# Performance work log

Hardware: AMD Instinct MI355X
Metric: run time of the kernel (lower is better)

The kernel has to match this reference:

```python
import jax, jax.numpy as jnp
import numpy as np

ALPHA = 1.702  # sigmoid-GLU scale
LIMIT = 7.0    # clamp limit
TOP_K = 2      # num_experts_per_tok


def setup_inputs() -> dict:
    key = jax.random.key(0)
    ks = jax.random.split(key, 4)
    B, S, H, E, I = 2, 1024, 1024, 8, 2048
    return {
        "hidden_states": jax.random.normal(ks[0], (B, S, H), jnp.float32),
        "router_weight": jax.random.normal(ks[1], (E, H), jnp.float32),
        "router_bias": jnp.zeros((E,), jnp.float32),
        "gate_up_proj": jax.random.normal(ks[2], (E, H, 2 * I), jnp.float32) * 0.02,
        "gate_up_bias": jnp.zeros((E, 2 * I), jnp.float32),
        "down_proj": jax.random.normal(ks[3], (E, I, H), jnp.float32) * 0.02,
        "down_bias": jnp.zeros((E, H), jnp.float32),
    }


def reference(hidden_states, router_weight, router_bias, gate_up_proj,
              gate_up_bias, down_proj, down_bias):
    B, S, H = hidden_states.shape
    E, _, two_I = gate_up_proj.shape
    I = two_I // 2

    flat = hidden_states.reshape(B * S, H)  # [T, H]

    # Router: softmax + top-k
    logits = flat @ router_weight.T + router_bias            # [T, E]
    scores = jax.nn.softmax(logits, axis=-1)
    topk_w, topk_idx = jax.lax.top_k(scores, TOP_K)          # [T, K]

    # Dense per-expert gated FFN (einsum 'abmh,ehn->abemn' computes all experts
    # on all tokens; the reshape/permute dance is a mathematical no-op).
    gu = jnp.einsum('th,ehn->ten', flat, gate_up_proj) + gate_up_bias  # [T, E, 2I]
    gate = jnp.minimum(gu[..., :I], LIMIT)
    up = jnp.clip(gu[..., I:], -LIMIT, LIMIT)
    glu = gate * jax.nn.sigmoid(gate * ALPHA)
    act = (up + 1.0) * glu                                   # [T, E, I]

    down = jnp.einsum('tei,eih->teh', act, down_proj) + down_bias  # [T, E, H]

    # Combine: gather each token's top-k expert outputs, weighted sum.
    gathered = jnp.take_along_axis(down, topk_idx[:, :, None], axis=1)  # [T, K, H]
    out = (gathered * topk_w[:, :, None]).sum(axis=1)        # [T, H]
    return out.reshape(B, S, H)
```

## Files before the change

### kernel.cpp

```cpp
#include <hip/hip_runtime.h>
#include <math.h>

#define TT 2048
#define HH 1024
#define EE 8
#define II 2048
#define N1 4096
#define ALPHA 1.702f
#define LIMIT 7.0f

typedef __attribute__((ext_vector_type(8))) short short8;
typedef __attribute__((ext_vector_type(4))) float floatx4;

__device__ __forceinline__ short f2bf(float f) {
  union { float f; unsigned u; } v; v.f = f;
  unsigned r = (v.u + 0x7fffu + ((v.u >> 16) & 1u)) >> 16;
  return (short)r;
}
__device__ __forceinline__ float bf2f(unsigned short s) {
  union { unsigned u; float f; } v; v.u = ((unsigned)s) << 16;
  return v.f;
}

__global__ __launch_bounds__(256) void router_kernel(
    const float* __restrict__ x, const float* __restrict__ rw,
    const float* __restrict__ rb, int* __restrict__ topk_idx,
    float* __restrict__ topk_w) {
  const int t = blockIdx.x;
  const float* xr = x + (size_t)t * HH;
  const int lane = threadIdx.x & 63;
  const int wave = threadIdx.x >> 6;
  float xv[16];
#pragma unroll
  for (int i = 0; i < 16; i++) xv[i] = xr[lane + i * 64];
  __shared__ float logits[EE];
#pragma unroll
  for (int ee = 0; ee < 2; ee++) {
    const int e = wave * 2 + ee;
    const float* wr = rw + (size_t)e * HH;
    float s = 0.f;
#pragma unroll
    for (int i = 0; i < 16; i++) s += xv[i] * wr[lane + i * 64];
#pragma unroll
    for (int off = 32; off > 0; off >>= 1) s += __shfl_down(s, off, 64);
    if (lane == 0) logits[e] = s + rb[e];
  }
  __syncthreads();
  if (threadIdx.x == 0) {
    float l[EE], sc[EE];
    float mx = -3.4e38f;
    for (int i = 0; i < EE; i++) { l[i] = logits[i]; mx = fmaxf(mx, l[i]); }
    float sum = 0.f;
    for (int i = 0; i < EE; i++) { sc[i] = expf(l[i] - mx); sum += sc[i]; }
    const float inv = 1.f / sum;
    int i0 = 0;
    for (int i = 1; i < EE; i++) if (sc[i] > sc[i0]) i0 = i;
    int i1 = (i0 == 0) ? 1 : 0;
    for (int i = 0; i < EE; i++) if (i != i0 && sc[i] > sc[i1]) i1 = i;
    topk_idx[t * 2 + 0] = i0;
    topk_idx[t * 2 + 1] = i1;
    topk_w[t * 2 + 0] = sc[i0] * inv;
    topk_w[t * 2 + 1] = sc[i1] * inv;
  }
}

__global__ void assign_kernel(const int* __restrict__ topk_idx,
                              int* __restrict__ counts, int* __restrict__ rows) {
  const int id = blockIdx.x * blockDim.x + threadIdx.x;
  if (id >= TT * 2) return;
  const int e = topk_idx[id];
  const int slot = atomicAdd(&counts[e], 1);
  rows[e * TT + slot] = id;
}

__global__ __launch_bounds__(256) void gemm_gu(
    const float* __restrict__ x, const float* __restrict__ gup,
    const float* __restrict__ gub, const int* __restrict__ counts,
    const int* __restrict__ rows, unsigned short* __restrict__ gu) {
  const int e = blockIdx.z, mtile = blockIdx.y, ntile = blockIdx.x;
  const int count = counts[e];
  if (mtile * 128 >= count) return;
  const int* rl = rows + e * TT + mtile * 128;
  __shared__ short As[128][40];
  __shared__ short Bs[128][40];
  const int tid = threadIdx.x;
  const int lane = tid & 63, wave = tid >> 6;
  const int wm = (wave & 1) << 6, wn = (wave >> 1) << 6;
  const int quad = lane >> 4, r16 = lane & 15;

  const int arow = tid >> 2, akoct = tid & 3;
  const int cr0 = (mtile * 128 + arow < count) ? arow : (count - 1 - mtile * 128);
  const int cr1 = (mtile * 128 + arow + 64 < count) ? arow + 64 : (count - 1 - mtile * 128);
  const float* a0 = x + (size_t)(rl[cr0] >> 1) * HH;
  const float* a1 = x + (size_t)(rl[cr1] >> 1) * HH;

  const int bn = tid & 127, bk = tid >> 7;
  const float* bb = gup + (size_t)e * HH * N1 + ntile * 128 + bn;

  floatx4 acc[4][4] = {};

  for (int k0 = 0; k0 < HH; k0 += 32) {
    __syncthreads();
    {
      const float4* p = (const float4*)(a0 + k0 + akoct * 8);
      float4 v0 = p[0], v1 = p[1];
      short8 s;
      s[0]=f2bf(v0.x); s[1]=f2bf(v0.y); s[2]=f2bf(v0.z); s[3]=f2bf(v0.w);
      s[4]=f2bf(v1.x); s[5]=f2bf(v1.y); s[6]=f2bf(v1.z); s[7]=f2bf(v1.w);
      *(short8*)&As[arow][akoct * 8] = s;
      p = (const float4*)(a1 + k0 + akoct * 8);
      v0 = p[0]; v1 = p[1];
      s[0]=f2bf(v0.x); s[1]=f2bf(v0.y); s[2]=f2bf(v0.z); s[3]=f2bf(v0.w);
      s[4]=f2bf(v1.x); s[5]=f2bf(v1.y); s[6]=f2bf(v1.z); s[7]=f2bf(v1.w);
      *(short8*)&As[arow + 64][akoct * 8] = s;
    }
    {
      const float* p = bb + (size_t)(k0 + bk * 8) * N1;
      short8 s;
#pragma unroll
      for (int j = 0; j < 8; j++) s[j] = f2bf(p[(size_t)j * N1]);
      *(short8*)&Bs[bn][bk * 8] = s;
      p = bb + (size_t)(k0 + (bk + 2) * 8) * N1;
#pragma unroll
      for (int j = 0; j < 8; j++) s[j] = f2bf(p[(size_t)j * N1]);
      *(short8*)&Bs[bn][(bk + 2) * 8] = s;
    }
    __syncthreads();
    short8 af[4], bf_[4];
#pragma unroll
    for (int i = 0; i < 4; i++)
      af[i] = *(const short8*)&As[wm + i * 16 + r16][quad * 8];
#pragma unroll
    for (int j = 0; j < 4; j++)
      bf_[j] = *(const short8*)&Bs[wn + j * 16 + r16][quad * 8];
#pragma unroll
    for (int i = 0; i < 4; i++)
#pragma unroll
      for (int j = 0; j < 4; j++)
        acc[i][j] = __builtin_amdgcn_mfma_f32_16x16x32_bf16(af[i], bf_[j], acc[i][j], 0, 0, 0);
  }
#pragma unroll
  for (int i = 0; i < 4; i++) {
#pragma unroll
    for (int reg = 0; reg < 4; reg++) {
      const int rrow = wm + i * 16 + quad * 4 + reg;
      if (mtile * 128 + rrow < count) {
        const int ent = rl[rrow];
        unsigned short* orow = gu + (size_t)ent * N1 + ntile * 128;
#pragma unroll
        for (int j = 0; j < 4; j++) {
          const int c = wn + j * 16 + r16;
          const float v = acc[i][j][reg] + gub[e * N1 + ntile * 128 + c];
          orow[c] = (unsigned short)f2bf(v);
        }
      }
    }
  }
}

__global__ void act_kernel(const unsigned short* __restrict__ gu,
                           unsigned short* __restrict__ act) {
  const int id = blockIdx.x * blockDim.x + threadIdx.x;
  if (id >= TT * 2 * II) return;
  const int r = id >> 11;
  const int i = id & (II - 1);
  float g = bf2f(gu[(size_t)r * N1 + i]);
  float u = bf2f(gu[(size_t)r * N1 + II + i]);
  g = fminf(g, LIMIT);
  u = fminf(fmaxf(u, -LIMIT), LIMIT);
  const float glu = g / (1.f + expf(-g * ALPHA));
  act[(size_t)r * II + i] = (unsigned short)f2bf((u + 1.f) * glu);
}

__global__ __launch_bounds__(256) void gemm_down(
    const unsigned short* __restrict__ act, const float* __restrict__ dp,
    const float* __restrict__ db, const int* __restrict__ counts,
    const int* __restrict__ rows, float* __restrict__ dout) {
  const int e = blockIdx.z, mtile = blockIdx.y, ntile = blockIdx.x;
  const int count = counts[e];
  if (mtile * 128 >= count) return;
  const int* rl = rows + e * TT + mtile * 128;
  __shared__ short As[128][40];
  __shared__ short Bs[128][40];
  const int tid = threadIdx.x;
  const int lane = tid & 63, wave = tid >> 6;
  const int wm = (wave & 1) << 6, wn = (wave >> 1) << 6;
  const int quad = lane >> 4, r16 = lane & 15;

  const int arow = tid >> 2, akoct = tid & 3;
  const int cr0 = (mtile * 128 + arow < count) ? arow : (count - 1 - mtile * 128);
  const int cr1 = (mtile * 128 + arow + 64 < count) ? arow + 64 : (count - 1 - mtile * 128);
  const unsigned short* a0 = act + (size_t)rl[cr0] * II;
  const unsigned short* a1 = act + (size_t)rl[cr1] * II;

  const int bn = tid & 127, bk = tid >> 7;
  const float* bb = dp + (size_t)e * II * HH + ntile * 128 + bn;

  floatx4 acc[4][4] = {};

  for (int k0 = 0; k0 < II; k0 += 32) {
    __syncthreads();
    {
      *(short8*)&As[arow][akoct * 8] = *(const short8*)(a0 + k0 + akoct * 8);
      *(short8*)&As[arow + 64][akoct * 8] = *(const short8*)(a1 + k0 + akoct * 8);
    }
    {
      const float* p = bb + (size_t)(k0 + bk * 8) * HH;
      short8 s;
#pragma unroll
      for (int j = 0; j < 8; j++) s[j] = f2bf(p[(size_t)j * HH]);
      *(short8*)&Bs[bn][bk * 8] = s;
      p = bb + (size_t)(k0 + (bk + 2) * 8) * HH;
#pragma unroll
      for (int j = 0; j < 8; j++) s[j] = f2bf(p[(size_t)j * HH]);
      *(short8*)&Bs[bn][(bk + 2) * 8] = s;
    }
    __syncthreads();
    short8 af[4], bf_[4];
#pragma unroll
    for (int i = 0; i < 4; i++)
      af[i] = *(const short8*)&As[wm + i * 16 + r16][quad * 8];
#pragma unroll
    for (int j = 0; j < 4; j++)
      bf_[j] = *(const short8*)&Bs[wn + j * 16 + r16][quad * 8];
#pragma unroll
    for (int i = 0; i < 4; i++)
#pragma unroll
      for (int j = 0; j < 4; j++)
        acc[i][j] = __builtin_amdgcn_mfma_f32_16x16x32_bf16(af[i], bf_[j], acc[i][j], 0, 0, 0);
  }
#pragma unroll
  for (int i = 0; i < 4; i++) {
#pragma unroll
    for (int reg = 0; reg < 4; reg++) {
      const int rrow = wm + i * 16 + quad * 4 + reg;
      if (mtile * 128 + rrow < count) {
        const int ent = rl[rrow];
        float* orow = dout + (size_t)ent * HH + ntile * 128;
#pragma unroll
        for (int j = 0; j < 4; j++) {
          const int c = wn + j * 16 + r16;
          orow[c] = acc[i][j][reg] + db[e * HH + ntile * 128 + c];
        }
      }
    }
  }
}

__global__ void combine_kernel(const float* __restrict__ dout,
                               const float* __restrict__ tw,
                               float* __restrict__ out) {
  const int id = blockIdx.x * blockDim.x + threadIdx.x;
  const int t = id >> 8;
  const int h = (id & 255) * 4;
  const float w0 = tw[t * 2], w1 = tw[t * 2 + 1];
  const float4 a = *(const float4*)(dout + (size_t)(2 * t) * HH + h);
  const float4 b = *(const float4*)(dout + (size_t)(2 * t + 1) * HH + h);
  float4 o;
  o.x = w0 * a.x + w1 * b.x;
  o.y = w0 * a.y + w1 * b.y;
  o.z = w0 * a.z + w1 * b.z;
  o.w = w0 * a.w + w1 * b.w;
  *(float4*)(out + (size_t)t * HH + h) = o;
}

extern "C" void kernel_launch(void* const* d_in, const int* in_sizes, int n_in,
                              void* d_out, int out_size, void* d_ws, size_t ws_size,
                              hipStream_t stream) {
  const float* x   = (const float*)d_in[0];
  const float* rw  = (const float*)d_in[1];
  const float* rb  = (const float*)d_in[2];
  const float* gup = (const float*)d_in[3];
  const float* gub = (const float*)d_in[4];
  const float* dp  = (const float*)d_in[5];
  const float* db  = (const float*)d_in[6];
  float* out = (float*)d_out;

  char* ws = (char*)d_ws;
  int*   topk_idx = (int*)(ws + 0);
  float* topk_w   = (float*)(ws + 16384);
  int*   counts   = (int*)(ws + 32768);
  int*   rows     = (int*)(ws + 33024);
  unsigned short* gu  = (unsigned short*)(ws + 131072);
  unsigned short* act = (unsigned short*)(ws + 131072 + 33554432);
  float* dout = (float*)(ws + 131072 + 33554432 + 16777216);

  router_kernel<<<TT, 256, 0, stream>>>(x, rw, rb, topk_idx, topk_w);
  hipMemsetAsync(counts, 0, 64, stream);
  assign_kernel<<<(TT * 2 + 255) / 256, 256, 0, stream>>>(topk_idx, counts, rows);
  gemm_gu<<<dim3(N1 / 128, TT / 128, EE), 256, 0, stream>>>(x, gup, gub, counts, rows, gu);
  act_kernel<<<(TT * 2 * II) / 256, 256, 0, stream>>>(gu, act);
  gemm_down<<<dim3(HH / 128, TT / 128, EE), 256, 0, stream>>>(act, dp, db, counts, rows, dout);
  combine_kernel<<<(TT * HH / 4) / 256, 256, 0, stream>>>(dout, topk_w, out);
}
```

Measured before the change: 454.3 us.

## Pre-transpose weights to bf16, pipeline GEMMs with async LDS loads, fuse activation

Adds kernels that convert x to bf16 and transpose both expert weight tensors into K-contiguous bf16 layouts each call. The GEMMs then stage tiles with global_load_lds in a double-buffered pipeline, avoiding strided fp32 loads and per-element conversion. gemm_gu now pairs gate and up columns in one tile and applies the GLU activation in its epilogue, which removes act_kernel and the gu intermediate. gemm_down splits K four ways into separate partial buffers that combine_kernel sums, trading more combine traffic for more parallel blocks. The per-call weight transpose adds memory traffic of its own.

```diff
diff --git a/kernel.cpp b/kernel.cpp
--- a/kernel.cpp
+++ b/kernel.cpp
@@ -11,15 +11,64 @@
 
 typedef __attribute__((ext_vector_type(8))) short short8;
 typedef __attribute__((ext_vector_type(4))) float floatx4;
+typedef __attribute__((ext_vector_type(4))) unsigned int uintx4;
 
 __device__ __forceinline__ short f2bf(float f) {
   union { float f; unsigned u; } v; v.f = f;
   unsigned r = (v.u + 0x7fffu + ((v.u >> 16) & 1u)) >> 16;
   return (short)r;
 }
-__device__ __forceinline__ float bf2f(unsigned short s) {
-  union { unsigned u; float f; } v; v.u = ((unsigned)s) << 16;
-  return v.f;
+__device__ __forceinline__ unsigned cvt2(float lo, float hi) {
+  unsigned r;
+  asm("v_cvt_pk_bf16_f32 %0, %1, %2" : "=v"(r) : "v"(lo), "v"(hi));
+  return r;
+}
+__device__ __forceinline__ void gload16(const void* g, void* l) {
+  __builtin_amdgcn_global_load_lds(
+      (const __attribute__((address_space(1))) unsigned int*)g,
+      (__attribute__((address_space(3))) unsigned int*)l, 16, 0, 0);
+}
+
+__global__ __launch_bounds__(256) void convert_x(const float* __restrict__ x,
+                                                 unsigned short* __restrict__ xb) {
+  const int id = blockIdx.x * 256 + threadIdx.x;
+  const float4 a = ((const float4*)x)[id * 2];
+  const float4 b = ((const float4*)x)[id * 2 + 1];
+  uintx4 w;
+  w[0] = cvt2(a.x, a.y); w[1] = cvt2(a.z, a.w);
+  w[2] = cvt2(b.x, b.y); w[3] = cvt2(b.z, b.w);
+  ((uintx4*)xb)[id] = w;
+}
+
+__global__ __launch_bounds__(256) void transpose_bf16(
+    const float* __restrict__ src, unsigned short* __restrict__ dst,
+    const int K, const int N) {
+  const int e = blockIdx.z;
+  const int n0 = blockIdx.x * 64, k0 = blockIdx.y * 64;
+  __shared__ float tile[64][68];
+  const float* s = src + (size_t)e * K * N;
+  unsigned short* d = dst + (size_t)e * N * K;
+  const int t = threadIdx.x;
+  const int nq = t & 15, kr = t >> 4;
+#pragma unroll
+  for (int r = 0; r < 4; r++) {
+    const int k = r * 16 + kr;
+    const float4 v = *(const float4*)(s + (size_t)(k0 + k) * N + n0 + nq * 4);
+    tile[k][nq * 4 + 0] = v.x; tile[k][nq * 4 + 1] = v.y;
+    tile[k][nq * 4 + 2] = v.z; tile[k][nq * 4 + 3] = v.w;
+  }
+  __syncthreads();
+  const int n = t >> 2, ks = (t & 3) * 16;
+  unsigned short* orow = d + (size_t)(n0 + n) * K + k0 + ks;
+  uintx4 w0, w1;
+#pragma unroll
+  for (int m = 0; m < 4; m++)
+    w0[m] = cvt2(tile[ks + 2 * m][n], tile[ks + 2 * m + 1][n]);
+#pragma unroll
+  for (int m = 0; m < 4; m++)
+    w1[m] = cvt2(tile[ks + 8 + 2 * m][n], tile[ks + 9 + 2 * m][n]);
+  *(uintx4*)orow = w0;
+  *(uintx4*)(orow + 8) = w1;
 }
 
 __global__ __launch_bounds__(256) void router_kernel(
@@ -73,178 +122,219 @@
   rows[e * TT + slot] = id;
 }
 
-__global__ __launch_bounds__(256) void gemm_gu(
-    const float* __restrict__ x, const float* __restrict__ gup,
+__global__ __launch_bounds__(256, 4) void gemm_gu(
+    const unsigned short* __restrict__ xb, const unsigned short* __restrict__ gupt,
     const float* __restrict__ gub, const int* __restrict__ counts,
-    const int* __restrict__ rows, unsigned short* __restrict__ gu) {
+    const int* __restrict__ rows, unsigned short* __restrict__ act) {
   const int e = blockIdx.z, mtile = blockIdx.y, ntile = blockIdx.x;
   const int count = counts[e];
   if (mtile * 128 >= count) return;
   const int* rl = rows + e * TT + mtile * 128;
-  __shared__ short As[128][40];
-  __shared__ short Bs[128][40];
+  __shared__ __align__(16) char smem[33280];
+  unsigned short* As = (unsigned short*)smem;
+  unsigned short* Bs = (unsigned short*)(smem + 16384);
+  float* glds = (float*)smem;
   const int tid = threadIdx.x;
   const int lane = tid & 63, wave = tid >> 6;
   const int wm = (wave & 1) << 6, wn = (wave >> 1) << 6;
   const int quad = lane >> 4, r16 = lane & 15;
 
-  const int arow = tid >> 2, akoct = tid & 3;
-  const int cr0 = (mtile * 128 + arow < count) ? arow : (count - 1 - mtile * 128);
-  const int cr1 = (mtile * 128 + arow + 64 < count) ? arow + 64 : (count - 1 - mtile * 128);
-  const float* a0 = x + (size_t)(rl[cr0] >> 1) * HH;
-  const float* a1 = x + (size_t)(rl[cr1] >> 1) * HH;
-
-  const int bn = tid & 127, bk = tid >> 7;
-  const float* bb = gup + (size_t)e * HH * N1 + ntile * 128 + bn;
+  const int lrow = lane >> 2, lko = (lane & 3) * 8;
+  const int q0 = wave * 2, q1 = q0 + 1;
+  const int row0 = q0 * 16 + lrow, row1 = q1 * 16 + lrow;
+  const int last = count - 1 - mtile * 128;
+  const int cr0 = row0 <= last ? row0 : last;
+  const int cr1 = row1 <= last ? row1 : last;
+  const unsigned short* pA0 = xb + (size_t)(rl[cr0] >> 1) * HH + lko;
+  const unsigned short* pA1 = xb + (size_t)(rl[cr1] >> 1) * HH + lko;
+  const int bn0 = (row0 < 64) ? (ntile * 64 + row0) : (II + ntile * 64 + row0 - 64);
+  const int bn1 = (row1 < 64) ? (ntile * 64 + row1) : (II + ntile * 64 + row1 - 64);
+  const unsigned short* pB0 = gupt + (size_t)e * N1 * HH + (size_t)bn0 * HH + lko;
+  const unsigned short* pB1 = gupt + (size_t)e * N1 * HH + (size_t)bn1 * HH + lko;
+  unsigned short* dA0 = As + q0 * 512;
+  unsigned short* dA1 = As + q1 * 512;
+  unsigned short* dB0 = Bs + q0 * 512;
+  unsigned short* dB1 = Bs + q1 * 512;
 
   floatx4 acc[4][4] = {};
-
-  for (int k0 = 0; k0 < HH; k0 += 32) {
-    __syncthreads();
-    {
-      const float4* p = (const float4*)(a0 + k0 + akoct * 8);
-      float4 v0 = p[0], v1 = p[1];
-      short8 s;
-      s[0]=f2bf(v0.x); s[1]=f2bf(v0.y); s[2]=f2bf(v0.z); s[3]=f2bf(v0.w);
-      s[4]=f2bf(v1.x); s[5]=f2bf(v1.y); s[6]=f2bf(v1.z); s[7]=f2bf(v1.w);
-      *(short8*)&As[arow][akoct * 8] = s;
-      p = (const float4*)(a1 + k0 + akoct * 8);
-      v0 = p[0]; v1 = p[1];
-      s[0]=f2bf(v0.x); s[1]=f2bf(v0.y); s[2]=f2bf(v0.z); s[3]=f2bf(v0.w);
-      s[4]=f2bf(v1.x); s[5]=f2bf(v1.y); s[6]=f2bf(v1.z); s[7]=f2bf(v1.w);
-      *(short8*)&As[arow + 64][akoct * 8] = s;
+  const int NTK = HH / 32;
+
+#define STAGE(B, kk) do { \
+    const int ko_ = (kk) * 32; \
+    gload16(pA0 + ko_, dA0 + (B) * 4096); \
+    gload16(pA1 + ko_, dA1 + (B) * 4096); \
+    gload16(pB0 + ko_, dB0 + (B) * 4096); \
+    gload16(pB1 + ko_, dB1 + (B) * 4096); \
+  } while (0)
+
+#define PHASE(B) do { \
+    asm volatile("s_waitcnt vmcnt(4)" ::: "memory"); \
+    __builtin_amdgcn_s_barrier(); \
+    short8 af[4], bf4[4]; \
+    _Pragma("unroll") for (int i = 0; i < 4; i++) \
+      af[i] = *(const short8*)(As + (B) * 4096 + (wm + i * 16 + r16) * 32 + quad * 8); \
+    _Pragma("unroll") for (int j = 0; j < 4; j++) \
+      bf4[j] = *(const short8*)(Bs + (B) * 4096 + (wn + j * 16 + r16) * 32 + quad * 8); \
+    asm volatile("s_waitcnt lgkmcnt(0)" ::: "memory"); \
+    __builtin_amdgcn_sched_barrier(0); \
+    __builtin_amdgcn_s_barrier(); \
+    { const int ks_ = kn < NTK ? kn : NTK - 1; kn++; STAGE(B, ks_); } \
+    __builtin_amdgcn_sched_barrier(0); \
+    __builtin_amdgcn_s_setprio(1); \
+    _Pragma("unroll") for (int i = 0; i < 4; i++) \
+      _Pragma("unroll") for (int j = 0; j < 4; j++) \
+        acc[i][j] = __builtin_amdgcn_mfma_f32_16x16x32_bf16(af[i], bf4[j], acc[i][j], 0, 0, 0); \
+    __builtin_amdgcn_s_setprio(0); \
+  } while (0)
+
+  STAGE(0, 0);
+  STAGE(1, 1);
+  int kn = 2;
+#pragma unroll 1
+  for (int t = 0; t < NTK; t += 2) {
+    PHASE(0);
+    PHASE(1);
+  }
+  asm volatile("s_waitcnt vmcnt(0)" ::: "memory");
+  __builtin_amdgcn_s_barrier();
+
+  const int colbase = ntile * 64;
+  if (wn == 0) {
+#pragma unroll
+    for (int j = 0; j < 4; j++) {
+      const int c = j * 16 + r16;
+      const float gb = gub[e * N1 + colbase + c];
+#pragma unroll
+      for (int i = 0; i < 4; i++)
+#pragma unroll
+        for (int reg = 0; reg < 4; reg++) {
+          const int rr = wm + i * 16 + quad * 4 + reg;
+          float g = acc[i][j][reg] + gb;
+          g = fminf(g, LIMIT);
+          glds[rr * 65 + c] = g / (1.f + expf(-g * ALPHA));
+        }
     }
-    {
-      const float* p = bb + (size_t)(k0 + bk * 8) * N1;
-      short8 s;
-#pragma unroll
-      for (int j = 0; j < 8; j++) s[j] = f2bf(p[(size_t)j * N1]);
-      *(short8*)&Bs[bn][bk * 8] = s;
-      p = bb + (size_t)(k0 + (bk + 2) * 8) * N1;
-#pragma unroll
-      for (int j = 0; j < 8; j++) s[j] = f2bf(p[(size_t)j * N1]);
-      *(short8*)&Bs[bn][(bk + 2) * 8] = s;
+  }
+  __builtin_amdgcn_s_barrier();
+  if (wn == 64) {
+#pragma unroll
+    for (int j = 0; j < 4; j++) {
+      const int c = j * 16 + r16;
+      const float ub = gub[e * N1 + II + colbase + c];
+#pragma unroll
+      for (int i = 0; i < 4; i++)
+#pragma unroll
+        for (int reg = 0; reg < 4; reg++) {
+          const int rr = wm + i * 16 + quad * 4 + reg;
+          if (mtile * 128 + rr < count) {
+            float u = acc[i][j][reg] + ub;
+            u = fminf(fmaxf(u, -LIMIT), LIMIT);
+            const float glu = glds[rr * 65 + c];
+            act[(size_t)rl[rr] * II + colbase + c] = (unsigned short)f2bf((u + 1.f) * glu);
+          }
+        }
     }
-    __syncthreads();
-    short8 af[4], bf_[4];
-#pragma unroll
-    for (int i = 0; i < 4; i++)
-      af[i] = *(const short8*)&As[wm + i * 16 + r16][quad * 8];
-#pragma unroll
-    for (int j = 0; j < 4; j++)
-      bf_[j] = *(const short8*)&Bs[wn + j * 16 + r16][quad * 8];
-#pragma unroll
-    for (int i = 0; i < 4; i++)
-#pragma unroll
-      for (int j = 0; j < 4; j++)
-        acc[i][j] = __builtin_amdgcn_mfma_f32_16x16x32_bf16(af[i], bf_[j], acc[i][j], 0, 0, 0);
-  }
-#pragma unroll
-  for (int i = 0; i < 4; i++) {
-#pragma unroll
-    for (int reg = 0; reg < 4; reg++) {
-      const int rrow = wm + i * 16 + quad * 4 + reg;
-      if (mtile * 128 + rrow < count) {
-        const int ent = rl[rrow];
-        unsigned short* orow = gu + (size_t)ent * N1 + ntile * 128;
-#pragma unroll
-        for (int j = 0; j < 4; j++) {
-          const int c = wn + j * 16 + r16;
-          const float v = acc[i][j][reg] + gub[e * N1 + ntile * 128 + c];
-          orow[c] = (unsigned short)f2bf(v);
-        }
-      }
-    }
-  }
-}
-
-__global__ void act_kernel(const unsigned short* __restrict__ gu,
-                           unsigned short* __restrict__ act) {
-  const int id = blockIdx.x * blockDim.x + threadIdx.x;
-  if (id >= TT * 2 * II) return;
-  const int r = id >> 11;
-  const int i = id & (II - 1);
-  float g = bf2f(gu[(size_t)r * N1 + i]);
-  float u = bf2f(gu[(size_t)r * N1 + II + i]);
-  g = fminf(g, LIMIT);
-  u = fminf(fmaxf(u, -LIMIT), LIMIT);
-  const float glu = g / (1.f + expf(-g * ALPHA));
-  act[(size_t)r * II + i] = (unsigned short)f2bf((u + 1.f) * glu);
-}
-
-__global__ __launch_bounds__(256) void gemm_down(
-    const unsigned short* __restrict__ act, const float* __restrict__ dp,
+  }
+#undef STAGE
+#undef PHASE
+}
+
+__global__ __launch_bounds__(256, 4) void gemm_down(
+    const unsigned short* __restrict__ act, const unsigned short* __restrict__ dpt,
     const float* __restrict__ db, const int* __restrict__ counts,
     const int* __restrict__ rows, float* __restrict__ dout) {
-  const int e = blockIdx.z, mtile = blockIdx.y, ntile = blockIdx.x;
+  const int e = blockIdx.z >> 2, kc = blockIdx.z & 3;
+  const int mtile = blockIdx.y, ntile = blockIdx.x;
   const int count = counts[e];
   if (mtile * 128 >= count) return;
+  const int kb = kc * (II / 4);
   const int* rl = rows + e * TT + mtile * 128;
-  __shared__ short As[128][40];
-  __shared__ short Bs[128][40];
+  __shared__ __align__(16) char smem[32768];
+  unsigned short* As = (unsigned short*)smem;
+  unsigned short* Bs = (unsigned short*)(smem + 16384);
   const int tid = threadIdx.x;
   const int lane = tid & 63, wave = tid >> 6;
   const int wm = (wave & 1) << 6, wn = (wave >> 1) << 6;
   const int quad = lane >> 4, r16 = lane & 15;
 
-  const int arow = tid >> 2, akoct = tid & 3;
-  const int cr0 = (mtile * 128 + arow < count) ? arow : (count - 1 - mtile * 128);
-  const int cr1 = (mtile * 128 + arow + 64 < count) ? arow + 64 : (count - 1 - mtile * 128);
-  const unsigned short* a0 = act + (size_t)rl[cr0] * II;
-  const unsigned short* a1 = act + (size_t)rl[cr1] * II;
-
-  const int bn = tid & 127, bk = tid >> 7;
-  const float* bb = dp + (size_t)e * II * HH + ntile * 128 + bn;
+  const int lrow = lane >> 2, lko = (lane & 3) * 8;
+  const int q0 = wave * 2, q1 = q0 + 1;
+  const int row0 = q0 * 16 + lrow, row1 = q1 * 16 + lrow;
+  const int last = count - 1 - mtile * 128;
+  const int cr0 = row0 <= last ? row0 : last;
+  const int cr1 = row1 <= last ? row1 : last;
+  const unsigned short* pA0 = act + (size_t)rl[cr0] * II + kb + lko;
+  const unsigned short* pA1 = act + (size_t)rl[cr1] * II + kb + lko;
+  const unsigned short* pB0 = dpt + (size_t)e * HH * II + (size_t)(ntile * 128 + row0) * II + kb + lko;
+  const unsigned short* pB1 = dpt + (size_t)e * HH * II + (size_t)(ntile * 128 + row1) * II + kb + lko;
+  unsigned short* dA0 = As + q0 * 512;
+  unsigned short* dA1 = As + q1 * 512;
+  unsigned short* dB0 = Bs + q0 * 512;
+  unsigned short* dB1 = Bs + q1 * 512;
 
   floatx4 acc[4][4] = {};
-
-  for (int k0 = 0; k0 < II; k0 += 32) {
-    __syncthreads();
-    {
-      *(short8*)&As[arow][akoct * 8] = *(const short8*)(a0 + k0 + akoct * 8);
-      *(short8*)&As[arow + 64][akoct * 8] = *(const short8*)(a1 + k0 + akoct * 8);
-    }
-    {
-      const float* p = bb + (size_t)(k0 + bk * 8) * HH;
-      short8 s;
-#pragma unroll
-      for (int j = 0; j < 8; j++) s[j] = f2bf(p[(size_t)j * HH]);
-      *(short8*)&Bs[bn][bk * 8] = s;
-      p = bb + (size_t)(k0 + (bk + 2) * 8) * HH;
-#pragma unroll
-      for (int j = 0; j < 8; j++) s[j] = f2bf(p[(size_t)j * HH]);
-      *(short8*)&Bs[bn][(bk + 2) * 8] = s;
-    }
-    __syncthreads();
-    short8 af[4], bf_[4];
-#pragma unroll
-    for (int i = 0; i < 4; i++)
-      af[i] = *(const short8*)&As[wm + i * 16 + r16][quad * 8];
-#pragma unroll
-    for (int j = 0; j < 4; j++)
-      bf_[j] = *(const short8*)&Bs[wn + j * 16 + r16][quad * 8];
-#pragma unroll
-    for (int i = 0; i < 4; i++)
-#pragma unroll
-      for (int j = 0; j < 4; j++)
-        acc[i][j] = __builtin_amdgcn_mfma_f32_16x16x32_bf16(af[i], bf_[j], acc[i][j], 0, 0, 0);
-  }
+  const int NTK = (II / 4) / 32;
+
+#define STAGE(B, kk) do { \
+    const int ko_ = (kk) * 32; \
+    gload16(pA0 + ko_, dA0 + (B) * 4096); \
+    gload16(pA1 + ko_, dA1 + (B) * 4096); \
+    gload16(pB0 + ko_, dB0 + (B) * 4096); \
+    gload16(pB1 + ko_, dB1 + (B) * 4096); \
+  } while (0)
+
+#define PHASE(B) do { \
+    asm volatile("s_waitcnt vmcnt(4)" ::: "memory"); \
+    __builtin_amdgcn_s_barrier(); \
+    short8 af[4], bf4[4]; \
+    _Pragma("unroll") for (int i = 0; i < 4; i++) \
+      af[i] = *(const short8*)(As + (B) * 4096 + (wm + i * 16 + r16) * 32 + quad * 8); \
+    _Pragma("unroll") for (int j = 0; j < 4; j++) \
+      bf4[j] = *(const short8*)(Bs + (B) * 4096 + (wn + j * 16 + r16) * 32 + quad * 8); \
+    asm volatile("s_waitcnt lgkmcnt(0)" ::: "memory"); \
+    __builtin_amdgcn_sched_barrier(0); \
+    __builtin_amdgcn_s_barrier(); \
+    { const int ks_ = kn < NTK ? kn : NTK - 1; kn++; STAGE(B, ks_); } \
+    __builtin_amdgcn_sched_barrier(0); \
+    __builtin_amdgcn_s_setprio(1); \
+    _Pragma("unroll") for (int i = 0; i < 4; i++) \
+      _Pragma("unroll") for (int j = 0; j < 4; j++) \
+        acc[i][j] = __builtin_amdgcn_mfma_f32_16x16x32_bf16(af[i], bf4[j], acc[i][j], 0, 0, 0); \
+    __builtin_amdgcn_s_setprio(0); \
+  } while (0)
+
+  STAGE(0, 0);
+  STAGE(1, 1);
+  int kn = 2;
+#pragma unroll 1
+  for (int t = 0; t < NTK; t += 2) {
+    PHASE(0);
+    PHASE(1);
+  }
+  asm volatile("s_waitcnt vmcnt(0)" ::: "memory");
+  __builtin_amdgcn_s_barrier();
+
+  float* dc = dout + (size_t)kc * ((size_t)TT * 2 * HH);
 #pragma unroll
   for (int i = 0; i < 4; i++) {
 #pragma unroll
     for (int reg = 0; reg < 4; reg++) {
-      const int rrow = wm + i * 16 + quad * 4 + reg;
-      if (mtile * 128 + rrow < count) {
-        const int ent = rl[rrow];
-        float* orow = dout + (size_t)ent * HH + ntile * 128;
+      const int rr = wm + i * 16 + quad * 4 + reg;
+      if (mtile * 128 + rr < count) {
+        const int ent = rl[rr];
+        float* orow = dc + (size_t)ent * HH + ntile * 128;
 #pragma unroll
         for (int j = 0; j < 4; j++) {
           const int c = wn + j * 16 + r16;
-          orow[c] = acc[i][j][reg] + db[e * HH + ntile * 128 + c];
+          float v = acc[i][j][reg];
+          if (kc == 0) v += db[e * HH + ntile * 128 + c];
+          orow[c] = v;
         }
       }
     }
   }
+#undef STAGE
+#undef PHASE
 }
 
 __global__ void combine_kernel(const float* __restrict__ dout,
@@ -254,8 +344,17 @@
   const int t = id >> 8;
   const int h = (id & 255) * 4;
   const float w0 = tw[t * 2], w1 = tw[t * 2 + 1];
-  const float4 a = *(const float4*)(dout + (size_t)(2 * t) * HH + h);
-  const float4 b = *(const float4*)(dout + (size_t)(2 * t + 1) * HH + h);
+  const size_t CH = (size_t)TT * 2 * HH;
+  const size_t r0 = (size_t)(2 * t) * HH + h;
+  const size_t r1 = (size_t)(2 * t + 1) * HH + h;
+  float4 a = {0.f, 0.f, 0.f, 0.f}, b = {0.f, 0.f, 0.f, 0.f};
+#pragma unroll
+  for (int c = 0; c < 4; c++) {
+    const float4 va = *(const float4*)(dout + c * CH + r0);
+    const float4 vb = *(const float4*)(dout + c * CH + r1);
+    a.x += va.x; a.y += va.y; a.z += va.z; a.w += va.w;
+    b.x += vb.x; b.y += vb.y; b.z += vb.z; b.w += vb.w;
+  }
   float4 o;
   o.x = w0 * a.x + w1 * b.x;
   o.y = w0 * a.y + w1 * b.y;
@@ -281,15 +380,19 @@
   float* topk_w   = (float*)(ws + 16384);
   int*   counts   = (int*)(ws + 32768);
   int*   rows     = (int*)(ws + 33024);
-  unsigned short* gu  = (unsigned short*)(ws + 131072);
-  unsigned short* act = (unsigned short*)(ws + 131072 + 33554432);
-  float* dout = (float*)(ws + 131072 + 33554432 + 16777216);
-
+  unsigned short* xb   = (unsigned short*)(ws + 131072);
+  unsigned short* gupt = (unsigned short*)(ws + 4325376);
+  unsigned short* dpt  = (unsigned short*)(ws + 71434240);
+  unsigned short* act  = (unsigned short*)(ws + 104988672);
+  float* dout = (float*)(ws + 4325376);
+
+  convert_x<<<TT * HH / 8 / 256, 256, 0, stream>>>(x, xb);
+  transpose_bf16<<<dim3(N1 / 64, HH / 64, EE), 256, 0, stream>>>(gup, gupt, HH, N1);
+  transpose_bf16<<<dim3(HH / 64, II / 64, EE), 256, 0, stream>>>(dp, dpt, II, HH);
   router_kernel<<<TT, 256, 0, stream>>>(x, rw, rb, topk_idx, topk_w);
   hipMemsetAsync(counts, 0, 64, stream);
   assign_kernel<<<(TT * 2 + 255) / 256, 256, 0, stream>>>(topk_idx, counts, rows);
-  gemm_gu<<<dim3(N1 / 128, TT / 128, EE), 256, 0, stream>>>(x, gup, gub, counts, rows, gu);
-  act_kernel<<<(TT * 2 * II) / 256, 256, 0, stream>>>(gu, act);
-  gemm_down<<<dim3(HH / 128, TT / 128, EE), 256, 0, stream>>>(act, dp, db, counts, rows, dout);
+  gemm_gu<<<dim3(II / 64, TT / 128, EE), 256, 0, stream>>>(xb, gupt, gub, counts, rows, act);
+  gemm_down<<<dim3(HH / 128, TT / 128, EE * 4), 256, 0, stream>>>(act, dpt, db, counts, rows, dout);
   combine_kernel<<<(TT * HH / 4) / 256, 256, 0, stream>>>(dout, topk_w, out);
 }
```

New measurement: 429.1 us. 5.6% less time.
